# Kernel optimization log

Hardware: AMD Instinct MI355X
Metric: run time of the kernel (lower is better)

## Reference

```python
import jax, jax.numpy as jnp
import numpy as np

# constants from init_kwargs
NUM_ITERS = 3
NUM_SLOTS = 8
INPUT_SIZE = 64
SLOT_SIZE = 64
MLP_HIDDEN = 128
EPS = 1e-8
NUM_HEADS = 4
HEAD_DIM = SLOT_SIZE // NUM_HEADS

B = 64
N_KV = 8192


def layernorm(x, g, b):
    m = jnp.mean(x, axis=-1, keepdims=True)
    v = jnp.mean((x - m) ** 2, axis=-1, keepdims=True)
    return (x - m) * jax.lax.rsqrt(v + 1e-5) * g + b


def setup_inputs() -> dict:
    key = jax.random.key(0)
    ks = jax.random.split(key, 16)
    s = 0.02
    return {
        "inputs": jax.random.normal(ks[0], (B, N_KV, INPUT_SIZE), jnp.float32),
        "slots": jax.random.normal(ks[1], (B, NUM_SLOTS, SLOT_SIZE), jnp.float32),
        "ln_in_g": jnp.ones((INPUT_SIZE,), jnp.float32),
        "ln_in_b": jnp.zeros((INPUT_SIZE,), jnp.float32),
        "ln_slot_g": jnp.ones((SLOT_SIZE,), jnp.float32),
        "ln_slot_b": jnp.zeros((SLOT_SIZE,), jnp.float32),
        "ln_mlp_g": jnp.ones((SLOT_SIZE,), jnp.float32),
        "ln_mlp_b": jnp.zeros((SLOT_SIZE,), jnp.float32),
        "Wq": jax.random.normal(ks[2], (SLOT_SIZE, SLOT_SIZE), jnp.float32) * s,
        "Wk": jax.random.normal(ks[3], (INPUT_SIZE, SLOT_SIZE), jnp.float32) * s,
        "Wv": jax.random.normal(ks[4], (INPUT_SIZE, SLOT_SIZE), jnp.float32) * s,
        "W_ih": jax.random.normal(ks[5], (3 * SLOT_SIZE, SLOT_SIZE), jnp.float32) * s,
        "W_hh": jax.random.normal(ks[6], (3 * SLOT_SIZE, SLOT_SIZE), jnp.float32) * s,
        "b_ih": jnp.zeros((3 * SLOT_SIZE,), jnp.float32),
        "b_hh": jnp.zeros((3 * SLOT_SIZE,), jnp.float32),
        "mlp_W1": jax.random.normal(ks[7], (SLOT_SIZE, MLP_HIDDEN), jnp.float32) * s,
        "mlp_b1": jnp.zeros((MLP_HIDDEN,), jnp.float32),
        "mlp_W2": jax.random.normal(ks[8], (MLP_HIDDEN, SLOT_SIZE), jnp.float32) * s,
        "mlp_b2": jnp.zeros((SLOT_SIZE,), jnp.float32),
    }


def gru_cell(x, h, W_ih, W_hh, b_ih, b_hh):
    # torch.nn.GRUCell math
    gx = x @ W_ih.T + b_ih  # [..., 3D]
    gh = h @ W_hh.T + b_hh
    xr, xz, xn = jnp.split(gx, 3, axis=-1)
    hr, hz, hn = jnp.split(gh, 3, axis=-1)
    r = jax.nn.sigmoid(xr + hr)
    z = jax.nn.sigmoid(xz + hz)
    n = jnp.tanh(xn + r * hn)
    return (1.0 - z) * n + z * h


def reference(inputs, slots, ln_in_g, ln_in_b, ln_slot_g, ln_slot_b, ln_mlp_g, ln_mlp_b,
              Wq, Wk, Wv, W_ih, W_hh, b_ih, b_hh, mlp_W1, mlp_b1, mlp_W2, mlp_b2):
    b, n_kv, _ = inputs.shape
    n_q = slots.shape[1]
    x = layernorm(inputs, ln_in_g, ln_in_b)
    k = (x @ Wk).reshape(b, n_kv, NUM_HEADS, HEAD_DIM).transpose(0, 2, 1, 3)  # [B,H,Nkv,Dh]
    v = (x @ Wv).reshape(b, n_kv, NUM_HEADS, HEAD_DIM).transpose(0, 2, 1, 3)
    k = k * (HEAD_DIM ** -0.5)
    attn_vis = None
    for _ in range(NUM_ITERS):
        slots_prev = slots
        s = layernorm(slots, ln_slot_g, ln_slot_b)
        q = (s @ Wq).reshape(b, n_q, NUM_HEADS, HEAD_DIM).transpose(0, 2, 1, 3)  # [B,H,Nq,Dh]
        logits = jnp.einsum('bhnd,bhqd->bhnq', k, q)  # [B,H,Nkv,Nq]
        # softmax jointly over (heads * slots) per kv token
        lt = logits.transpose(0, 2, 1, 3).reshape(b, n_kv, NUM_HEADS * n_q)
        attn = jax.nn.softmax(lt, axis=-1).reshape(b, n_kv, NUM_HEADS, n_q).transpose(0, 2, 1, 3)  # [B,H,Nkv,Nq]
        attn_vis = attn.sum(axis=1)  # [B,Nkv,Nq]
        attn = attn + EPS
        attn = attn / jnp.sum(attn, axis=-2, keepdims=True)  # normalize over Nkv
        updates = jnp.einsum('bhnq,bhnd->bqhd', attn, v).reshape(b, n_q, SLOT_SIZE)
        slots = gru_cell(updates, slots_prev, W_ih, W_hh, b_ih, b_hh)
        h = jax.nn.relu(layernorm(slots, ln_mlp_g, ln_mlp_b) @ mlp_W1 + mlp_b1)
        slots = slots + (h @ mlp_W2 + mlp_b2)
    return slots, attn_vis
```

## Files before the change

### kernel.cpp

```cpp
#include <hip/hip_runtime.h>

#define NKV 8192
#define NB 64

typedef __attribute__((ext_vector_type(8))) short short8;
typedef __attribute__((ext_vector_type(8))) unsigned short ushort8;
typedef __attribute__((ext_vector_type(4))) unsigned short usx4;
typedef __attribute__((ext_vector_type(4))) float f32x4;

__device__ __forceinline__ float bf2f(unsigned short u) {
  return __uint_as_float(((unsigned int)u) << 16);
}
__device__ __forceinline__ unsigned short f2bf(float f) {
  unsigned int x = __float_as_uint(f);
  return (unsigned short)((x + 0x7fffu + ((x >> 16) & 1u)) >> 16);
}
__device__ __forceinline__ float sigm(float x) { return 1.f / (1.f + __expf(-x)); }

__global__ __launch_bounds__(256) void k_wprep(
    const float* __restrict__ Wk, const float* __restrict__ Wv,
    unsigned short* __restrict__ wf) {
  int idx = blockIdx.x * 256 + threadIdx.x;
  int lane = idx & 63, ct = (idx >> 6) & 7, kf = idx >> 9;
  int half = lane >> 4, rlo = lane & 15;
  const float* W = (ct < 4) ? Wk : Wv;
  int cc = (ct & 3) * 16 + rlo;
  ushort8 pk;
#pragma unroll
  for (int i = 0; i < 8; ++i)
    pk[i] = f2bf(W[(kf * 32 + half * 8 + i) * 64 + cc]);
  *(ushort8*)(wf + (size_t)idx * 8) = pk;
}

__global__ __launch_bounds__(256) void k_proj(
    const float* __restrict__ x, const float* __restrict__ gin,
    const float* __restrict__ bin, const unsigned short* __restrict__ wf,
    unsigned short* __restrict__ kv) {
  const int lane = threadIdx.x & 63;
  const int wave = threadIdx.x >> 6;
  const int half = lane >> 4, rlo = lane & 15;

  short8 bfr[2][8];
  const ushort8* wf8 = (const ushort8*)wf;
#pragma unroll
  for (int kf = 0; kf < 2; ++kf)
#pragma unroll
    for (int ct = 0; ct < 8; ++ct)
      bfr[kf][ct] = (short8)wf8[(kf * 8 + ct) * 64 + lane];

  float g0[8], g1[8], bb0[8], bb1[8];
#pragma unroll
  for (int i = 0; i < 8; ++i) {
    g0[i] = gin[half * 8 + i];      bb0[i] = bin[half * 8 + i];
    g1[i] = gin[32 + half * 8 + i]; bb1[i] = bin[32 + half * 8 + i];
  }
  long tok0 = ((long)blockIdx.x * 4 + wave) * 128;
  for (int tile = 0; tile < 8; ++tile) {
    long row = tok0 + tile * 16 + rlo;
    const f32x4* p4 = (const f32x4*)(x + row * 64);
    f32x4 u0 = p4[half * 2], u1 = p4[half * 2 + 1];
    f32x4 u2 = p4[8 + half * 2], u3 = p4[9 + half * 2];
    float s = 0.f, ss = 0.f;
#pragma unroll
    for (int i = 0; i < 4; ++i) {
      s += u0[i] + u1[i] + u2[i] + u3[i];
      ss = fmaf(u0[i], u0[i], fmaf(u1[i], u1[i], fmaf(u2[i], u2[i], fmaf(u3[i], u3[i], ss))));
    }
    s += __shfl_xor(s, 16); ss += __shfl_xor(ss, 16);
    s += __shfl_xor(s, 32); ss += __shfl_xor(ss, 32);
    float m = s * 0.015625f;
    float var = ss * 0.015625f - m * m;
    float rs = rsqrtf(var + 1e-5f);
    short8 a0, a1;
#pragma unroll
    for (int i = 0; i < 4; ++i) {
      a0[i]     = (short)f2bf((u0[i] - m) * rs * g0[i]     + bb0[i]);
      a0[i + 4] = (short)f2bf((u1[i] - m) * rs * g0[i + 4] + bb0[i + 4]);
      a1[i]     = (short)f2bf((u2[i] - m) * rs * g1[i]     + bb1[i]);
      a1[i + 4] = (short)f2bf((u3[i] - m) * rs * g1[i + 4] + bb1[i + 4]);
    }
    long t = tok0 + tile * 16 + rlo;
#pragma unroll
    for (int ct = 0; ct < 8; ++ct) {
      f32x4 acc = {0.f, 0.f, 0.f, 0.f};
      acc = __builtin_amdgcn_mfma_f32_16x16x32_bf16(bfr[0][ct], a0, acc, 0, 0, 0);
      acc = __builtin_amdgcn_mfma_f32_16x16x32_bf16(bfr[1][ct], a1, acc, 0, 0, 0);
      float sc = (ct < 4) ? 0.25f : 1.f;
      usx4 pk;
#pragma unroll
      for (int r = 0; r < 4; ++r) pk[r] = f2bf(acc[r] * sc);
      *(usx4*)(kv + t * 128 + ct * 16 + half * 4) = pk;
    }
  }
}

__global__ __launch_bounds__(64) void k_prep(
    const float* __restrict__ slots_in, const float* __restrict__ g_slot,
    const float* __restrict__ b_slot, const float* __restrict__ Wq,
    float* __restrict__ slots_buf, float* __restrict__ qbuf,
    float* __restrict__ Sg, float* __restrict__ Wg) {
  int b = blockIdx.x >> 3, s = blockIdx.x & 7, d = threadIdx.x;
  __shared__ float l2_s[64];
  float x = slots_in[(b * 8 + s) * 64 + d];
  slots_buf[(b * 8 + s) * 64 + d] = x;
  float sum = x, sq = x * x;
#pragma unroll
  for (int msk = 1; msk < 64; msk <<= 1) { sum += __shfl_xor(sum, msk); sq += __shfl_xor(sq, msk); }
  float mean = sum * 0.015625f, var = sq * 0.015625f - mean * mean;
  float ln = (x - mean) * rsqrtf(var + 1e-5f) * g_slot[d] + b_slot[d];
  l2_s[d] = ln;
  __syncthreads();
  float acc = 0.f;
#pragma unroll 8
  for (int j = 0; j < 64; ++j) acc = fmaf(l2_s[j], Wq[j * 64 + d], acc);
  acc *= 0.25f;
  int hh = d >> 4, dh = d & 15, hq = hh * 8 + s;
  qbuf[(b * 32 + hq) * 16 + dh] = acc;
  if (d < 4) Sg[b * 32 + d * 8 + s] = 0.f;
  Wg[(b * 32 + hq) * 16 + dh] = 0.f;
}

__global__ __launch_bounds__(64) void k_qfrag(
    const float* __restrict__ qbuf, unsigned short* __restrict__ qfrag) {
  int b = blockIdx.x, lane = threadIdx.x;
  int half = lane >> 4, rlo = lane & 15;
#pragma unroll
  for (int m = 0; m < 2; ++m) {
    int hq = m * 16 + rlo, h = hq >> 3;
#pragma unroll
    for (int kc = 0; kc < 2; ++kc) {
      ushort8 pk;
#pragma unroll
      for (int i = 0; i < 8; ++i) {
        int d = kc * 32 + half * 8 + i;
        float v = ((d >> 4) == h) ? qbuf[(b * 32 + hq) * 16 + (d & 15)] : 0.f;
        pk[i] = f2bf(v);
      }
      *(ushort8*)(qfrag + ((size_t)(b * 4 + m * 2 + kc) * 64 + lane) * 8) = pk;
    }
  }
}

template <int IT>
__global__ __launch_bounds__(256) void k_attn(
    const unsigned short* __restrict__ kv, const unsigned short* __restrict__ qfrag,
    float* __restrict__ Sg, float* __restrict__ Wg,
    float* __restrict__ vis) {
  constexpr bool last = (IT == 2);
  const int PS = 34;
  int b = blockIdx.x >> 5, chunk = blockIdx.x & 31;
  int lane = threadIdx.x & 63, wave = threadIdx.x >> 6;
  int half = lane >> 4, rlo = lane & 15;
  __shared__ unsigned short P[4][64 * PS];
  __shared__ float Wred[4][512];
  int t0 = chunk * 256 + wave * 64;

  short8 afr[2][2];
  const ushort8* qf8 = (const ushort8*)qfrag;
#pragma unroll
  for (int m = 0; m < 2; ++m)
#pragma unroll
    for (int kc = 0; kc < 2; ++kc)
      afr[m][kc] = (short8)qf8[(b * 4 + m * 2 + kc) * 64 + lane];

  float Sacc[2][4];
#pragma unroll
  for (int m = 0; m < 2; ++m)
#pragma unroll
    for (int r = 0; r < 4; ++r) Sacc[m][r] = 0.f;

#pragma unroll
  for (int nt = 0; nt < 4; ++nt) {
    long rowb = ((long)(b * NKV) + t0 + nt * 16 + rlo) * 128;
    short8 bk0 = *(const short8*)(kv + rowb + half * 8);
    short8 bk1 = *(const short8*)(kv + rowb + 32 + half * 8);
    f32x4 acc0 = {0.f, 0.f, 0.f, 0.f}, acc1 = {0.f, 0.f, 0.f, 0.f};
    acc0 = __builtin_amdgcn_mfma_f32_16x16x32_bf16(afr[0][0], bk0, acc0, 0, 0, 0);
    acc0 = __builtin_amdgcn_mfma_f32_16x16x32_bf16(afr[0][1], bk1, acc0, 0, 0, 0);
    acc1 = __builtin_amdgcn_mfma_f32_16x16x32_bf16(afr[1][0], bk0, acc1, 0, 0, 0);
    acc1 = __builtin_amdgcn_mfma_f32_16x16x32_bf16(afr[1][1], bk1, acc1, 0, 0, 0);
    float e0[4], e1[4], ssum = 0.f;
#pragma unroll
    for (int r = 0; r < 4; ++r) {
      e0[r] = __expf(acc0[r]); e1[r] = __expf(acc1[r]);
      ssum += e0[r] + e1[r];
    }
    ssum += __shfl_xor(ssum, 16);
    ssum += __shfl_xor(ssum, 32);
    float rs = __builtin_amdgcn_rcpf(ssum);
    float a0[4], a1[4];
#pragma unroll
    for (int r = 0; r < 4; ++r) {
      a0[r] = e0[r] * rs; a1[r] = e1[r] * rs;
      Sacc[0][r] += a0[r]; Sacc[1][r] += a1[r];
    }
    int off = (nt * 16 + rlo) * PS;
    unsigned int w00 = (unsigned int)f2bf(a0[0]) | ((unsigned int)f2bf(a0[1]) << 16);
    unsigned int w01 = (unsigned int)f2bf(a0[2]) | ((unsigned int)f2bf(a0[3]) << 16);
    unsigned int w10 = (unsigned int)f2bf(a1[0]) | ((unsigned int)f2bf(a1[1]) << 16);
    unsigned int w11 = (unsigned int)f2bf(a1[2]) | ((unsigned int)f2bf(a1[3]) << 16);
    *(unsigned int*)(&P[wave][off + half * 4])      = w00;
    *(unsigned int*)(&P[wave][off + half * 4 + 2])  = w01;
    *(unsigned int*)(&P[wave][off + 16 + half * 4]) = w10;
    *(unsigned int*)(&P[wave][off + 16 + half * 4 + 2]) = w11;
    if (last) {
      float vl[4];
#pragma unroll
      for (int r = 0; r < 4; ++r) {
        vl[r] = a0[r] + a1[r];
        vl[r] += __shfl_xor(vl[r], 32);
      }
      if (half < 2) {
        long tt = (long)b * NKV + t0 + nt * 16 + rlo;
#pragma unroll
        for (int r = 0; r < 4; ++r) vis[tt * 8 + (half & 1) * 4 + r] = vl[r];
      }
    }
  }
#pragma unroll
  for (int m = 0; m < 2; ++m)
#pragma unroll
    for (int r = 0; r < 4; ++r) {
      Sacc[m][r] += __shfl_xor(Sacc[m][r], 1);
      Sacc[m][r] += __shfl_xor(Sacc[m][r], 2);
      Sacc[m][r] += __shfl_xor(Sacc[m][r], 4);
      Sacc[m][r] += __shfl_xor(Sacc[m][r], 8);
    }
  if (rlo == 0) {
#pragma unroll
    for (int m = 0; m < 2; ++m)
#pragma unroll
      for (int r = 0; r < 4; ++r)
        atomicAdd(&Sg[b * 32 + m * 16 + half * 4 + r], Sacc[m][r]);
  }
#pragma unroll
  for (int h = 0; h < 4; ++h) {
    f32x4 wacc = {0.f, 0.f, 0.f, 0.f};
#pragma unroll
    for (int kc2 = 0; kc2 < 2; ++kc2) {
      short8 af, bf;
#pragma unroll
      for (int i = 0; i < 8; ++i) {
        af[i] = (short)P[wave][(kc2 * 32 + half * 8 + i) * PS + h * 8 + (rlo & 7)];
        bf[i] = (short)kv[((long)(b * NKV) + t0 + kc2 * 32 + half * 8 + i) * 128 + 64 + h * 16 + rlo];
      }
      wacc = __builtin_amdgcn_mfma_f32_16x16x32_bf16(af, bf, wacc, 0, 0, 0);
    }
    if (half < 2) {
#pragma unroll
      for (int r = 0; r < 4; ++r)
        Wred[wave][(h * 8 + half * 4 + r) * 16 + rlo] = wacc[r];
    }
  }
  __syncthreads();
  int tid = threadIdx.x;
#pragma unroll
  for (int r2 = 0; r2 < 2; ++r2) {
    int idx = tid + r2 * 256;
    atomicAdd(&Wg[b * 512 + idx],
              Wred[0][idx] + Wred[1][idx] + Wred[2][idx] + Wred[3][idx]);
  }
}

template <int IT>
__global__ __launch_bounds__(64) void k_update(
    float* __restrict__ Sg, float* __restrict__ Wg,
    float* __restrict__ slots_buf,
    const float* __restrict__ W_ih, const float* __restrict__ W_hh,
    const float* __restrict__ b_ih, const float* __restrict__ b_hh,
    const float* __restrict__ g_mlp, const float* __restrict__ b_mlp,
    const float* __restrict__ W1, const float* __restrict__ b1,
    const float* __restrict__ W2, const float* __restrict__ b2,
    const float* __restrict__ g_slot, const float* __restrict__ b_slot,
    const float* __restrict__ Wq, float* __restrict__ qbuf,
    float* __restrict__ out_slots) {
  constexpr int compute_next = (IT < 2);
  constexpr int write_out = (IT == 2);
  int b = blockIdx.x >> 3, s = blockIdx.x & 7, d = threadIdx.x;
  __shared__ float upd_s[64], h_s[64], lnm_s[64], h1_s[128], l2_s[64];
  float hp = slots_buf[(b * 8 + s) * 64 + d];
  int hh = d >> 4, dh = d & 15, hq = hh * 8 + s;
  float denom = Sg[b * 32 + hq] + 8192.f * 1e-8f;
  float updv = Wg[(b * 32 + hq) * 16 + dh] / denom;
  upd_s[d] = updv; h_s[d] = hp;
  __syncthreads();
  float xr = b_ih[d], xz = b_ih[64 + d], xn = b_ih[128 + d];
  float hr = b_hh[d], hz = b_hh[64 + d], hv3 = b_hh[128 + d];
  const float* wi0 = W_ih + d * 64;
  const float* wi1 = W_ih + (64 + d) * 64;
  const float* wi2 = W_ih + (128 + d) * 64;
  const float* wh0 = W_hh + d * 64;
  const float* wh1 = W_hh + (64 + d) * 64;
  const float* wh2 = W_hh + (128 + d) * 64;
#pragma unroll 4
  for (int jj = 0; jj < 16; ++jj) {
    f32x4 u = *(const f32x4*)&upd_s[jj * 4];
    f32x4 hvv = *(const f32x4*)&h_s[jj * 4];
    f32x4 a0 = *(const f32x4*)&wi0[jj * 4];
    f32x4 a1 = *(const f32x4*)&wi1[jj * 4];
    f32x4 a2 = *(const f32x4*)&wi2[jj * 4];
    f32x4 c0 = *(const f32x4*)&wh0[jj * 4];
    f32x4 c1 = *(const f32x4*)&wh1[jj * 4];
    f32x4 c2 = *(const f32x4*)&wh2[jj * 4];
#pragma unroll
    for (int i = 0; i < 4; ++i) {
      xr = fmaf(u[i], a0[i], xr);  xz = fmaf(u[i], a1[i], xz);  xn = fmaf(u[i], a2[i], xn);
      hr = fmaf(hvv[i], c0[i], hr); hz = fmaf(hvv[i], c1[i], hz); hv3 = fmaf(hvv[i], c2[i], hv3);
    }
  }
  float r = sigm(xr + hr);
  float z = sigm(xz + hz);
  float n = tanhf(xn + r * hv3);
  float hn = (1.f - z) * n + z * hp;
  float sum = hn, sq = hn * hn;
#pragma unroll
  for (int msk = 1; msk < 64; msk <<= 1) { sum += __shfl_xor(sum, msk); sq += __shfl_xor(sq, msk); }
  float mean = sum * 0.015625f, var = sq * 0.015625f - mean * mean;
  float lnv = (hn - mean) * rsqrtf(var + 1e-5f) * g_mlp[d] + b_mlp[d];
  lnm_s[d] = lnv;
  __syncthreads();
  float a1a = b1[d], a1b = b1[64 + d];
#pragma unroll 8
  for (int j = 0; j < 64; ++j) {
    float lj = lnm_s[j];
    a1a = fmaf(lj, W1[j * 128 + d], a1a);
    a1b = fmaf(lj, W1[j * 128 + 64 + d], a1b);
  }
  h1_s[d] = fmaxf(a1a, 0.f); h1_s[64 + d] = fmaxf(a1b, 0.f);
  __syncthreads();
  float a2 = b2[d];
#pragma unroll 8
  for (int c = 0; c < 128; ++c) a2 = fmaf(h1_s[c], W2[c * 64 + d], a2);
  float outv = hn + a2;
  slots_buf[(b * 8 + s) * 64 + d] = outv;
  if (write_out) out_slots[(b * 8 + s) * 64 + d] = outv;
  if (compute_next) {
    float sum2 = outv, sq2 = outv * outv;
#pragma unroll
    for (int msk = 1; msk < 64; msk <<= 1) { sum2 += __shfl_xor(sum2, msk); sq2 += __shfl_xor(sq2, msk); }
    float mean2 = sum2 * 0.015625f, var2 = sq2 * 0.015625f - mean2 * mean2;
    float l2 = (outv - mean2) * rsqrtf(var2 + 1e-5f) * g_slot[d] + b_slot[d];
    l2_s[d] = l2;
    __syncthreads();
    float acc = 0.f;
#pragma unroll 8
    for (int j = 0; j < 64; ++j) acc = fmaf(l2_s[j], Wq[j * 64 + d], acc);
    acc *= 0.25f;
    qbuf[(b * 32 + hq) * 16 + dh] = acc;
    if (d < 4) Sg[b * 32 + d * 8 + s] = 0.f;
    Wg[(b * 32 + hq) * 16 + dh] = 0.f;
  }
}

extern "C" void kernel_launch(void* const* d_in, const int* in_sizes, int n_in,
                              void* d_out, int out_size, void* d_ws, size_t ws_size,
                              hipStream_t stream) {
  const float* inputs    = (const float*)d_in[0];
  const float* slots     = (const float*)d_in[1];
  const float* ln_in_g   = (const float*)d_in[2];
  const float* ln_in_b   = (const float*)d_in[3];
  const float* ln_slot_g = (const float*)d_in[4];
  const float* ln_slot_b = (const float*)d_in[5];
  const float* ln_mlp_g  = (const float*)d_in[6];
  const float* ln_mlp_b  = (const float*)d_in[7];
  const float* Wq        = (const float*)d_in[8];
  const float* Wk        = (const float*)d_in[9];
  const float* Wv        = (const float*)d_in[10];
  const float* W_ih      = (const float*)d_in[11];
  const float* W_hh      = (const float*)d_in[12];
  const float* b_ih      = (const float*)d_in[13];
  const float* b_hh      = (const float*)d_in[14];
  const float* mlp_W1    = (const float*)d_in[15];
  const float* mlp_b1    = (const float*)d_in[16];
  const float* mlp_W2    = (const float*)d_in[17];
  const float* mlp_b2    = (const float*)d_in[18];

  float* out_slots = (float*)d_out;
  float* out_vis   = out_slots + 64 * 8 * 64;

  char* ws = (char*)d_ws;
  unsigned short* kv = (unsigned short*)ws;
  size_t off = (size_t)64 * 8192 * 128 * 2;
  float* qbuf      = (float*)(ws + off); off += (size_t)64 * 32 * 16 * 4;
  float* Sg        = (float*)(ws + off); off += (size_t)64 * 32 * 4;
  float* Wg        = (float*)(ws + off); off += (size_t)64 * 512 * 4;
  float* slots_buf = (float*)(ws + off); off += (size_t)64 * 512 * 4;
  unsigned short* wf = (unsigned short*)(ws + off); off += (size_t)1024 * 8 * 2;
  unsigned short* qfrag = (unsigned short*)(ws + off); off += (size_t)64 * 4 * 64 * 8 * 2;

  hipLaunchKernelGGL(k_wprep, dim3(4), dim3(256), 0, stream, Wk, Wv, wf);
  hipLaunchKernelGGL(k_proj, dim3(1024), dim3(256), 0, stream,
                     inputs, ln_in_g, ln_in_b, wf, kv);
  hipLaunchKernelGGL(k_prep, dim3(512), dim3(64), 0, stream,
                     slots, ln_slot_g, ln_slot_b, Wq, slots_buf, qbuf, Sg, Wg);
  hipLaunchKernelGGL(k_qfrag, dim3(64), dim3(64), 0, stream, qbuf, qfrag);

  hipLaunchKernelGGL((k_attn<0>), dim3(64 * 32), dim3(256), 0, stream,
                     kv, qfrag, Sg, Wg, out_vis);
  hipLaunchKernelGGL((k_update<0>), dim3(512), dim3(64), 0, stream,
                     Sg, Wg, slots_buf, W_ih, W_hh, b_ih, b_hh,
                     ln_mlp_g, ln_mlp_b, mlp_W1, mlp_b1, mlp_W2, mlp_b2,
                     ln_slot_g, ln_slot_b, Wq, qbuf, out_slots);
  hipLaunchKernelGGL(k_qfrag, dim3(64), dim3(64), 0, stream, qbuf, qfrag);
  hipLaunchKernelGGL((k_attn<1>), dim3(64 * 32), dim3(256), 0, stream,
                     kv, qfrag, Sg, Wg, out_vis);
  hipLaunchKernelGGL((k_update<1>), dim3(512), dim3(64), 0, stream,
                     Sg, Wg, slots_buf, W_ih, W_hh, b_ih, b_hh,
                     ln_mlp_g, ln_mlp_b, mlp_W1, mlp_b1, mlp_W2, mlp_b2,
                     ln_slot_g, ln_slot_b, Wq, qbuf, out_slots);
  hipLaunchKernelGGL(k_qfrag, dim3(64), dim3(64), 0, stream, qbuf, qfrag);
  hipLaunchKernelGGL((k_attn<2>), dim3(64 * 32), dim3(256), 0, stream,
                     kv, qfrag, Sg, Wg, out_vis);
  hipLaunchKernelGGL((k_update<2>), dim3(512), dim3(64), 0, stream,
                     Sg, Wg, slots_buf, W_ih, W_hh, b_ih, b_hh,
                     ln_mlp_g, ln_mlp_b, mlp_W1, mlp_b1, mlp_W2, mlp_b2,
                     ln_slot_g, ln_slot_b, Wq, qbuf, out_slots);
}
```

Measured before the change: 467.7 us.

## Stage V in LDS for attention, split projection grid, pre-transpose GRU weights

```diff
diff --git a/kernel.cpp b/kernel.cpp
--- a/kernel.cpp
+++ b/kernel.cpp
@@ -32,6 +32,17 @@
   *(ushort8*)(wf + (size_t)idx * 8) = pk;
 }
 
+__global__ __launch_bounds__(256) void k_gruprep(
+    const float* __restrict__ W_ih, const float* __restrict__ W_hh,
+    float* __restrict__ WihT, float* __restrict__ WhhT) {
+  int idx = blockIdx.x * 256 + threadIdx.x;
+  if (idx < 192 * 64) {
+    int o = idx >> 6, j = idx & 63;
+    WihT[j * 192 + o] = W_ih[idx];
+    WhhT[j * 192 + o] = W_hh[idx];
+  }
+}
+
 __global__ __launch_bounds__(256) void k_proj(
     const float* __restrict__ x, const float* __restrict__ gin,
     const float* __restrict__ bin, const unsigned short* __restrict__ wf,
@@ -54,8 +65,9 @@
     g0[i] = gin[half * 8 + i];      bb0[i] = bin[half * 8 + i];
     g1[i] = gin[32 + half * 8 + i]; bb1[i] = bin[32 + half * 8 + i];
   }
-  long tok0 = ((long)blockIdx.x * 4 + wave) * 128;
-  for (int tile = 0; tile < 8; ++tile) {
+  long tok0 = ((long)blockIdx.x * 4 + wave) * 32;
+#pragma unroll
+  for (int tile = 0; tile < 2; ++tile) {
     long row = tok0 + tile * 16 + rlo;
     const f32x4* p4 = (const f32x4*)(x + row * 64);
     f32x4 u0 = p4[half * 2], u1 = p4[half * 2 + 1];
@@ -147,13 +159,23 @@
     float* __restrict__ Sg, float* __restrict__ Wg,
     float* __restrict__ vis) {
   constexpr bool last = (IT == 2);
-  const int PS = 34;
   int b = blockIdx.x >> 5, chunk = blockIdx.x & 31;
   int lane = threadIdx.x & 63, wave = threadIdx.x >> 6;
   int half = lane >> 4, rlo = lane & 15;
-  __shared__ unsigned short P[4][64 * PS];
-  __shared__ float Wred[4][512];
+  __shared__ unsigned short P[4][64 * 34];
+  __shared__ unsigned short Vs[4][64 * 66];
   int t0 = chunk * 256 + wave * 64;
+  long gbase = ((long)(b * NKV) + t0) * 128;
+
+  {
+    int vtok = lane >> 3, vcol = (lane & 7) * 8;
+#pragma unroll
+    for (int r = 0; r < 8; ++r) {
+      int tr = r * 8 + vtok;
+      ushort8 vv = *(const ushort8*)(kv + gbase + (long)tr * 128 + 64 + vcol);
+      *(ushort8*)(&Vs[wave][tr * 66 + vcol]) = vv;
+    }
+  }
 
   short8 afr[2][2];
   const ushort8* qf8 = (const ushort8*)qfrag;
@@ -171,7 +193,7 @@
 
 #pragma unroll
   for (int nt = 0; nt < 4; ++nt) {
-    long rowb = ((long)(b * NKV) + t0 + nt * 16 + rlo) * 128;
+    long rowb = gbase + (long)(nt * 16 + rlo) * 128;
     short8 bk0 = *(const short8*)(kv + rowb + half * 8);
     short8 bk1 = *(const short8*)(kv + rowb + 32 + half * 8);
     f32x4 acc0 = {0.f, 0.f, 0.f, 0.f}, acc1 = {0.f, 0.f, 0.f, 0.f};
@@ -194,14 +216,14 @@
       a0[r] = e0[r] * rs; a1[r] = e1[r] * rs;
       Sacc[0][r] += a0[r]; Sacc[1][r] += a1[r];
     }
-    int off = (nt * 16 + rlo) * PS;
+    int off = (nt * 16 + rlo) * 34;
     unsigned int w00 = (unsigned int)f2bf(a0[0]) | ((unsigned int)f2bf(a0[1]) << 16);
     unsigned int w01 = (unsigned int)f2bf(a0[2]) | ((unsigned int)f2bf(a0[3]) << 16);
     unsigned int w10 = (unsigned int)f2bf(a1[0]) | ((unsigned int)f2bf(a1[1]) << 16);
     unsigned int w11 = (unsigned int)f2bf(a1[2]) | ((unsigned int)f2bf(a1[3]) << 16);
-    *(unsigned int*)(&P[wave][off + half * 4])      = w00;
-    *(unsigned int*)(&P[wave][off + half * 4 + 2])  = w01;
-    *(unsigned int*)(&P[wave][off + 16 + half * 4]) = w10;
+    *(unsigned int*)(&P[wave][off + half * 4])          = w00;
+    *(unsigned int*)(&P[wave][off + half * 4 + 2])      = w01;
+    *(unsigned int*)(&P[wave][off + 16 + half * 4])     = w10;
     *(unsigned int*)(&P[wave][off + 16 + half * 4 + 2]) = w11;
     if (last) {
       float vl[4];
@@ -233,23 +255,37 @@
       for (int r = 0; r < 4; ++r)
         atomicAdd(&Sg[b * 32 + m * 16 + half * 4 + r], Sacc[m][r]);
   }
+  short8 pa[2][2];
+#pragma unroll
+  for (int m = 0; m < 2; ++m)
+#pragma unroll
+    for (int kc = 0; kc < 2; ++kc) {
+      short8 f;
+#pragma unroll
+      for (int i = 0; i < 8; ++i)
+        f[i] = (short)P[wave][(kc * 32 + half * 8 + i) * 34 + m * 16 + rlo];
+      pa[m][kc] = f;
+    }
+  float* Wred = (float*)&P[wave][0];
+  int myh = half >> 1;
 #pragma unroll
   for (int h = 0; h < 4; ++h) {
-    f32x4 wacc = {0.f, 0.f, 0.f, 0.f};
-#pragma unroll
-    for (int kc2 = 0; kc2 < 2; ++kc2) {
-      short8 af, bf;
-#pragma unroll
-      for (int i = 0; i < 8; ++i) {
-        af[i] = (short)P[wave][(kc2 * 32 + half * 8 + i) * PS + h * 8 + (rlo & 7)];
-        bf[i] = (short)kv[((long)(b * NKV) + t0 + kc2 * 32 + half * 8 + i) * 128 + 64 + h * 16 + rlo];
+    short8 vb0, vb1;
+#pragma unroll
+    for (int i = 0; i < 8; ++i) {
+      vb0[i] = (short)Vs[wave][(half * 8 + i) * 66 + h * 16 + rlo];
+      vb1[i] = (short)Vs[wave][(32 + half * 8 + i) * 66 + h * 16 + rlo];
+    }
+#pragma unroll
+    for (int m = 0; m < 2; ++m) {
+      f32x4 wacc = {0.f, 0.f, 0.f, 0.f};
+      wacc = __builtin_amdgcn_mfma_f32_16x16x32_bf16(pa[m][0], vb0, wacc, 0, 0, 0);
+      wacc = __builtin_amdgcn_mfma_f32_16x16x32_bf16(pa[m][1], vb1, wacc, 0, 0, 0);
+      if (h == m * 2 + myh) {
+#pragma unroll
+        for (int r = 0; r < 4; ++r)
+          Wred[(m * 16 + half * 4 + r) * 16 + rlo] = wacc[r];
       }
-      wacc = __builtin_amdgcn_mfma_f32_16x16x32_bf16(af, bf, wacc, 0, 0, 0);
-    }
-    if (half < 2) {
-#pragma unroll
-      for (int r = 0; r < 4; ++r)
-        Wred[wave][(h * 8 + half * 4 + r) * 16 + rlo] = wacc[r];
     }
   }
   __syncthreads();
@@ -257,8 +293,9 @@
 #pragma unroll
   for (int r2 = 0; r2 < 2; ++r2) {
     int idx = tid + r2 * 256;
-    atomicAdd(&Wg[b * 512 + idx],
-              Wred[0][idx] + Wred[1][idx] + Wred[2][idx] + Wred[3][idx]);
+    float v = ((const float*)&P[0][0])[idx] + ((const float*)&P[1][0])[idx] +
+              ((const float*)&P[2][0])[idx] + ((const float*)&P[3][0])[idx];
+    atomicAdd(&Wg[b * 512 + idx], v);
   }
 }
 
@@ -266,7 +303,7 @@
 __global__ __launch_bounds__(64) void k_update(
     float* __restrict__ Sg, float* __restrict__ Wg,
     float* __restrict__ slots_buf,
-    const float* __restrict__ W_ih, const float* __restrict__ W_hh,
+    const float* __restrict__ WihT, const float* __restrict__ WhhT,
     const float* __restrict__ b_ih, const float* __restrict__ b_hh,
     const float* __restrict__ g_mlp, const float* __restrict__ b_mlp,
     const float* __restrict__ W1, const float* __restrict__ b1,
@@ -285,32 +322,20 @@
   upd_s[d] = updv; h_s[d] = hp;
   __syncthreads();
   float xr = b_ih[d], xz = b_ih[64 + d], xn = b_ih[128 + d];
-  float hr = b_hh[d], hz = b_hh[64 + d], hv3 = b_hh[128 + d];
-  const float* wi0 = W_ih + d * 64;
-  const float* wi1 = W_ih + (64 + d) * 64;
-  const float* wi2 = W_ih + (128 + d) * 64;
-  const float* wh0 = W_hh + d * 64;
-  const float* wh1 = W_hh + (64 + d) * 64;
-  const float* wh2 = W_hh + (128 + d) * 64;
-#pragma unroll 4
-  for (int jj = 0; jj < 16; ++jj) {
-    f32x4 u = *(const f32x4*)&upd_s[jj * 4];
-    f32x4 hvv = *(const f32x4*)&h_s[jj * 4];
-    f32x4 a0 = *(const f32x4*)&wi0[jj * 4];
-    f32x4 a1 = *(const f32x4*)&wi1[jj * 4];
-    f32x4 a2 = *(const f32x4*)&wi2[jj * 4];
-    f32x4 c0 = *(const f32x4*)&wh0[jj * 4];
-    f32x4 c1 = *(const f32x4*)&wh1[jj * 4];
-    f32x4 c2 = *(const f32x4*)&wh2[jj * 4];
-#pragma unroll
-    for (int i = 0; i < 4; ++i) {
-      xr = fmaf(u[i], a0[i], xr);  xz = fmaf(u[i], a1[i], xz);  xn = fmaf(u[i], a2[i], xn);
-      hr = fmaf(hvv[i], c0[i], hr); hz = fmaf(hvv[i], c1[i], hz); hv3 = fmaf(hvv[i], c2[i], hv3);
-    }
+  float hr = b_hh[d], hz = b_hh[64 + d], hn3 = b_hh[128 + d];
+#pragma unroll 8
+  for (int j = 0; j < 64; ++j) {
+    float uj = upd_s[j], hj = h_s[j];
+    xr = fmaf(uj, WihT[j * 192 + d], xr);
+    xz = fmaf(uj, WihT[j * 192 + 64 + d], xz);
+    xn = fmaf(uj, WihT[j * 192 + 128 + d], xn);
+    hr = fmaf(hj, WhhT[j * 192 + d], hr);
+    hz = fmaf(hj, WhhT[j * 192 + 64 + d], hz);
+    hn3 = fmaf(hj, WhhT[j * 192 + 128 + d], hn3);
   }
   float r = sigm(xr + hr);
   float z = sigm(xz + hz);
-  float n = tanhf(xn + r * hv3);
+  float n = tanhf(xn + r * hn3);
   float hn = (1.f - z) * n + z * hp;
   float sum = hn, sq = hn * hn;
 #pragma unroll
@@ -387,9 +412,12 @@
   float* slots_buf = (float*)(ws + off); off += (size_t)64 * 512 * 4;
   unsigned short* wf = (unsigned short*)(ws + off); off += (size_t)1024 * 8 * 2;
   unsigned short* qfrag = (unsigned short*)(ws + off); off += (size_t)64 * 4 * 64 * 8 * 2;
+  float* WihT = (float*)(ws + off); off += (size_t)192 * 64 * 4;
+  float* WhhT = (float*)(ws + off); off += (size_t)192 * 64 * 4;
 
   hipLaunchKernelGGL(k_wprep, dim3(4), dim3(256), 0, stream, Wk, Wv, wf);
-  hipLaunchKernelGGL(k_proj, dim3(1024), dim3(256), 0, stream,
+  hipLaunchKernelGGL(k_gruprep, dim3(48), dim3(256), 0, stream, W_ih, W_hh, WihT, WhhT);
+  hipLaunchKernelGGL(k_proj, dim3(4096), dim3(256), 0, stream,
                      inputs, ln_in_g, ln_in_b, wf, kv);
   hipLaunchKernelGGL(k_prep, dim3(512), dim3(64), 0, stream,
                      slots, ln_slot_g, ln_slot_b, Wq, slots_buf, qbuf, Sg, Wg);
@@ -398,21 +426,21 @@
   hipLaunchKernelGGL((k_attn<0>), dim3(64 * 32), dim3(256), 0, stream,
                      kv, qfrag, Sg, Wg, out_vis);
   hipLaunchKernelGGL((k_update<0>), dim3(512), dim3(64), 0, stream,
-                     Sg, Wg, slots_buf, W_ih, W_hh, b_ih, b_hh,
+                     Sg, Wg, slots_buf, WihT, WhhT, b_ih, b_hh,
                      ln_mlp_g, ln_mlp_b, mlp_W1, mlp_b1, mlp_W2, mlp_b2,
                      ln_slot_g, ln_slot_b, Wq, qbuf, out_slots);
   hipLaunchKernelGGL(k_qfrag, dim3(64), dim3(64), 0, stream, qbuf, qfrag);
   hipLaunchKernelGGL((k_attn<1>), dim3(64 * 32), dim3(256), 0, stream,
                      kv, qfrag, Sg, Wg, out_vis);
   hipLaunchKernelGGL((k_update<1>), dim3(512), dim3(64), 0, stream,
-                     Sg, Wg, slots_buf, W_ih, W_hh, b_ih, b_hh,
+                     Sg, Wg, slots_buf, WihT, WhhT, b_ih, b_hh,
                      ln_mlp_g, ln_mlp_b, mlp_W1, mlp_b1, mlp_W2, mlp_b2,
                      ln_slot_g, ln_slot_b, Wq, qbuf, out_slots);
   hipLaunchKernelGGL(k_qfrag, dim3(64), dim3(64), 0, stream, qbuf, qfrag);
   hipLaunchKernelGGL((k_attn<2>), dim3(64 * 32), dim3(256), 0, stream,
                      kv, qfrag, Sg, Wg, out_vis);
   hipLaunchKernelGGL((k_update<2>), dim3(512), dim3(64), 0, stream,
-                     Sg, Wg, slots_buf, W_ih, W_hh, b_ih, b_hh,
+                     Sg, Wg, slots_buf, WihT, WhhT, b_ih, b_hh,
                      ln_mlp_g, ln_mlp_b, mlp_W1, mlp_b1, mlp_W2, mlp_b2,
                      ln_slot_g, ln_slot_b, Wq, qbuf, out_slots);
 }
```

Result: no change. 467.1 us (-0.1%).
